# Kernel tuning notes

Hardware: AMD Instinct MI355X
Metric: run time of the kernel (lower is better)

Reference implementation:

```python
import jax, jax.numpy as jnp
import numpy as np

B, L, H, E = 2, 2048, 8, 64
S = L  # self-attention


def setup_inputs() -> dict:
    key = jax.random.key(0)
    k1, k2, k3, k4, k5 = jax.random.split(key, 5)
    return {
        "queries": jax.random.normal(k1, (B, L, H, E), dtype=jnp.float32),
        "keys": jax.random.normal(k2, (B, S, H, E), dtype=jnp.float32),
        "values": jax.random.normal(k3, (B, S, H, E), dtype=jnp.float32),
        "tau": jax.random.uniform(k4, (B, 1), dtype=jnp.float32),
        "delta": jax.random.normal(k5, (B, S), dtype=jnp.float32),
    }


def reference(queries, keys, values, tau, delta):
    # De-stationary attention: scores = (QK^T) * tau + delta, causal mask, softmax, AV
    E_ = queries.shape[-1]
    scale = 1.0 / jnp.sqrt(jnp.float32(E_))
    tau_b = tau[:, None, None, :]      # [B,1,1,1]
    delta_b = delta[:, None, None, :]  # [B,1,1,S]
    scores = jnp.einsum('blhe,bshe->bhls', queries, keys) * tau_b + delta_b  # [B,H,L,S]
    Lq, Sk = scores.shape[-2], scores.shape[-1]
    causal = jnp.triu(jnp.ones((Lq, Sk), dtype=bool), k=1)  # True = masked
    scores = jnp.where(causal[None, None], -jnp.inf, scores)
    A = jax.nn.softmax(scale * scores, axis=-1)
    V = jnp.einsum('bhls,bshd->blhd', A, values)
    return V
```

## Files before the change

### kernel.cpp

```cpp
#include <hip/hip_runtime.h>


typedef _Float16 h8 __attribute__((ext_vector_type(8)));
typedef _Float16 h2 __attribute__((ext_vector_type(2)));
typedef float f32x4 __attribute__((ext_vector_type(4)));

constexpr int Bc = 2, Lc = 2048, Hc = 8, Ec = 64, Sc = 2048;
constexpr int QTL = 128;
constexpr int NQT = Lc / QTL;
constexpr int KT = 64;
constexpr int LDK = 72;
constexpr float SCALE = 0.125f;
constexpr float LOG2E = 1.44269504088896340736f;

__device__ __forceinline__ h2 pk2(float x, float y) {
  return __builtin_bit_cast(h2, __builtin_amdgcn_cvt_pkrtz(x, y));
}
template <int CTRL>
__device__ __forceinline__ float dpp_f(float x) {
  int r = __builtin_amdgcn_update_dpp(0, __builtin_bit_cast(int, x), CTRL, 0xF, 0xF, true);
  return __builtin_bit_cast(float, r);
}
__device__ __forceinline__ float rowmax16(float x) {
  x = fmaxf(x, dpp_f<0xB1>(x));
  x = fmaxf(x, dpp_f<0x4E>(x));
  x = fmaxf(x, dpp_f<0x124>(x));
  x = fmaxf(x, dpp_f<0x128>(x));
  return x;
}

template <int CH_IT, int EPB>
__global__ __launch_bounds__(256, 2)
void dsattn_fwd(const float* __restrict__ Qg, const float* __restrict__ Kg,
                const float* __restrict__ Vg, const float* __restrict__ taug,
                const float* __restrict__ deltag, float* __restrict__ Og,
                _Float16* __restrict__ Opart, float* __restrict__ Mpart,
                float* __restrict__ Lpart) {
  __shared__ __align__(16) _Float16 Ks[2][KT * LDK];
  __shared__ __align__(16) _Float16 Vt[2][Ec * LDK];
  __shared__ __align__(16) _Float16 Pb[4][16 * LDK];

  int qt = NQT - 1, c0 = 0, pre_e = 0;
  if (CH_IT < 2 * NQT) {
    int bxx = (int)blockIdx.x;
#pragma unroll
    for (int q = NQT - 1; q >= 0; --q) {
      const int n = (2 * q + 1 + CH_IT) / CH_IT;
      if (bxx < n) { qt = q; c0 = bxx; break; }
      bxx -= n;
    }
#pragma unroll
    for (int q = 0; q < NQT; ++q)
      if (q < qt) pre_e += (2 * q + 1 + CH_IT) / CH_IT;
  } else {
    qt = NQT - 1 - (int)blockIdx.x;
  }
  const int ntiles = 2 * qt + 2;
  const int nch = (ntiles + CH_IT - 1) / CH_IT;
  const int ktBeg = c0 * CH_IT;
  const int ktEnd = min(ktBeg + CH_IT - 1, ntiles - 1);

  const int tid = threadIdx.x;
  const int wave = tid >> 6, lane = tid & 63;
  const int quad = lane >> 4, l16 = lane & 15;
  const int q0 = qt * QTL;
  const int bh = (int)blockIdx.y;
  const int b = bh >> 3, h = bh & 7;
  const float ct = taug[b] * (SCALE * LOG2E);

  h8 qfrag[2][2];
#pragma unroll
  for (int f = 0; f < 2; ++f)
#pragma unroll
    for (int kk = 0; kk < 2; ++kk) {
      const float* qp = Qg + (((size_t)b * Lc + q0 + 32 * wave + 16 * f + l16) * Hc + h) * Ec
                       + quad * 8 + kk * 32;
      const float4* p = (const float4*)qp;
      union { h8 v; h2 c[4]; } u;
      float4 a0 = p[0], a1 = p[1];
      u.c[0] = pk2(a0.x, a0.y); u.c[1] = pk2(a0.z, a0.w);
      u.c[2] = pk2(a1.x, a1.y); u.c[3] = pk2(a1.z, a1.w);
      qfrag[f][kk] = u.v;
    }

  h8 onesf;
#pragma unroll
  for (int j = 0; j < 8; ++j) onesf[j] = (_Float16)1.0f;

  f32x4 Oacc[2][4], Osum[2];
  float mrow[2][4];
#pragma unroll
  for (int f = 0; f < 2; ++f) {
#pragma unroll
    for (int nt = 0; nt < 4; ++nt) Oacc[f][nt] = (f32x4){0.f, 0.f, 0.f, 0.f};
    Osum[f] = (f32x4){0.f, 0.f, 0.f, 0.f};
#pragma unroll
    for (int r = 0; r < 4; ++r) mrow[f][r] = -1e30f;
  }

  const int srow = tid >> 2;
  const int sec = (tid & 3) << 4;
  const int vrp = ((tid >> 3) + 4 * (tid & 7)) & 31;
  const int ve8 = (tid & 7) << 3;

  _Float16* pb = &Pb[wave][0];
  const int lo = l16 & 1;
  const int pbase = (lo ? 32 : 0) + (l16 & ~1);
  float dcur[4];

  {
    const int kb = ktBeg * KT;
    const float* kp = Kg + (((size_t)b * Sc + kb + srow) * Hc + h) * Ec + sec;
    float4 c0v = ((const float4*)kp)[0], c1v = ((const float4*)kp)[1];
    float4 c2v = ((const float4*)kp)[2], c3v = ((const float4*)kp)[3];
    const float* vp0 = Vg + (((size_t)b * Sc + kb + 2 * vrp) * Hc + h) * Ec + ve8;
    const float* vp1 = vp0 + Hc * Ec;
    float4 r00 = ((const float4*)vp0)[0], r01 = ((const float4*)vp0)[1];
    float4 r10 = ((const float4*)vp1)[0], r11 = ((const float4*)vp1)[1];
#pragma unroll
    for (int nt = 0; nt < 4; ++nt)
      dcur[nt] = deltag[(size_t)b * Sc + kb + nt * 16 + l16] * (SCALE * LOG2E);
    union { h8 v; h2 c[4]; } w0, w1;
    w0.c[0] = pk2(c0v.x, c0v.y); w0.c[1] = pk2(c0v.z, c0v.w);
    w0.c[2] = pk2(c1v.x, c1v.y); w0.c[3] = pk2(c1v.z, c1v.w);
    w1.c[0] = pk2(c2v.x, c2v.y); w1.c[1] = pk2(c2v.z, c2v.w);
    w1.c[2] = pk2(c3v.x, c3v.y); w1.c[3] = pk2(c3v.z, c3v.w);
    *(h8*)&Ks[0][srow * LDK + sec] = w0.v;
    *(h8*)&Ks[0][srow * LDK + sec + 8] = w1.v;
    const float e0[8] = {r00.x, r00.y, r00.z, r00.w, r01.x, r01.y, r01.z, r01.w};
    const float e1[8] = {r10.x, r10.y, r10.z, r10.w, r11.x, r11.y, r11.z, r11.w};
#pragma unroll
    for (int j = 0; j < 8; ++j)
      *(h2*)&Vt[0][(ve8 + j) * LDK + 2 * vrp] = pk2(e0[j], e1[j]);
  }

  for (int kt = ktBeg; kt <= ktEnd; ++kt) {
    const int cur = (kt - ktBeg) & 1;
    const bool pf = (kt < ktEnd);
    const int kbase = kt * KT;

    __syncthreads();

    float4 kn0, kn1, kn2, kn3, vn00, vn01, vn10, vn11;
    float dn[4];
    if (pf) {
      const int nb = (kt + 1) * KT;
      const float* kp = Kg + (((size_t)b * Sc + nb + srow) * Hc + h) * Ec + sec;
      kn0 = ((const float4*)kp)[0]; kn1 = ((const float4*)kp)[1];
      kn2 = ((const float4*)kp)[2]; kn3 = ((const float4*)kp)[3];
      const float* vp0 = Vg + (((size_t)b * Sc + nb + 2 * vrp) * Hc + h) * Ec + ve8;
      const float* vp1 = vp0 + Hc * Ec;
      vn00 = ((const float4*)vp0)[0]; vn01 = ((const float4*)vp0)[1];
      vn10 = ((const float4*)vp1)[0]; vn11 = ((const float4*)vp1)[1];
#pragma unroll
      for (int nt = 0; nt < 4; ++nt)
        dn[nt] = deltag[(size_t)b * Sc + nb + nt * 16 + l16];
    }

    const int wtop = q0 + 32 * wave + 31;
    if (kbase <= wtop) {
      f32x4 Sacc[2][4];
#pragma unroll
      for (int f = 0; f < 2; ++f)
#pragma unroll
        for (int nt = 0; nt < 4; ++nt) Sacc[f][nt] = (f32x4){0.f, 0.f, 0.f, 0.f};
#pragma unroll
      for (int kk = 0; kk < 2; ++kk) {
        h8 bf[4];
#pragma unroll
        for (int nt = 0; nt < 4; ++nt)
          bf[nt] = *(const h8*)&Ks[cur][(nt * 16 + l16) * LDK + quad * 8 + kk * 32];
#pragma unroll
        for (int f = 0; f < 2; ++f)
#pragma unroll
          for (int nt = 0; nt < 4; ++nt)
            Sacc[f][nt] = __builtin_amdgcn_mfma_f32_16x16x32_f16(qfrag[f][kk], bf[nt], Sacc[f][nt], 0, 0, 0);
      }

#pragma unroll
      for (int f = 0; f < 2; ++f) {
        const int fr0 = q0 + 32 * wave + 16 * f;
        float sv[4][4];
#pragma unroll
        for (int nt = 0; nt < 4; ++nt)
#pragma unroll
          for (int r = 0; r < 4; ++r)
            sv[nt][r] = Sacc[f][nt][r] * ct + dcur[nt];
        if (kbase + 63 > fr0) {
#pragma unroll
          for (int nt = 0; nt < 4; ++nt) {
            const int key = kbase + nt * 16 + l16;
#pragma unroll
            for (int r = 0; r < 4; ++r)
              if (key > fr0 + quad * 4 + r) sv[nt][r] = -1e30f;
          }
        }
#pragma unroll
        for (int r = 0; r < 4; ++r) {
          float tm = fmaxf(fmaxf(sv[0][r], sv[1][r]), fmaxf(sv[2][r], sv[3][r]));
          tm = rowmax16(tm);
          float mn = fmaxf(mrow[f][r], tm);
          float alpha = __builtin_amdgcn_exp2f(mrow[f][r] - mn);
          mrow[f][r] = mn;
#pragma unroll
          for (int nt = 0; nt < 4; ++nt)
            sv[nt][r] = __builtin_amdgcn_exp2f(sv[nt][r] - mn);
          Osum[f][r] *= alpha;
#pragma unroll
          for (int nt = 0; nt < 4; ++nt) Oacc[f][nt][r] *= alpha;
        }
#pragma unroll
        for (int r = 0; r < 4; ++r) {
          float o0 = dpp_f<0xB1>(sv[0][r]);
          float o1 = dpp_f<0xB1>(sv[1][r]);
          float o2 = dpp_f<0xB1>(sv[2][r]);
          float o3 = dpp_f<0xB1>(sv[3][r]);
          h2 d0 = lo ? pk2(o2, sv[2][r]) : pk2(sv[0][r], o0);
          h2 d1 = lo ? pk2(o3, sv[3][r]) : pk2(sv[1][r], o1);
          _Float16* pp = &pb[((quad << 2) + r) * LDK + pbase];
          *(h2*)pp = d0;
          *(h2*)(pp + 16) = d1;
        }
        asm volatile("s_waitcnt lgkmcnt(0)" ::: "memory");

        h8 af0 = *(const h8*)&pb[l16 * LDK + quad * 8];
        h8 af1 = *(const h8*)&pb[l16 * LDK + quad * 8 + 32];

#pragma unroll
        for (int nt = 0; nt < 4; ++nt) {
          h8 vf0 = *(const h8*)&Vt[cur][(nt * 16 + l16) * LDK + quad * 8];
          Oacc[f][nt] = __builtin_amdgcn_mfma_f32_16x16x32_f16(af0, vf0, Oacc[f][nt], 0, 0, 0);
          h8 vf1 = *(const h8*)&Vt[cur][(nt * 16 + l16) * LDK + quad * 8 + 32];
          Oacc[f][nt] = __builtin_amdgcn_mfma_f32_16x16x32_f16(af1, vf1, Oacc[f][nt], 0, 0, 0);
        }
        Osum[f] = __builtin_amdgcn_mfma_f32_16x16x32_f16(af0, onesf, Osum[f], 0, 0, 0);
        Osum[f] = __builtin_amdgcn_mfma_f32_16x16x32_f16(af1, onesf, Osum[f], 0, 0, 0);
      }
    }

    if (pf) {
      _Float16* ksn = &Ks[cur ^ 1][0];
      _Float16* vtn = &Vt[cur ^ 1][0];
      union { h8 v; h2 c[4]; } w0, w1;
      w0.c[0] = pk2(kn0.x, kn0.y); w0.c[1] = pk2(kn0.z, kn0.w);
      w0.c[2] = pk2(kn1.x, kn1.y); w0.c[3] = pk2(kn1.z, kn1.w);
      w1.c[0] = pk2(kn2.x, kn2.y); w1.c[1] = pk2(kn2.z, kn2.w);
      w1.c[2] = pk2(kn3.x, kn3.y); w1.c[3] = pk2(kn3.z, kn3.w);
      *(h8*)&ksn[srow * LDK + sec] = w0.v;
      *(h8*)&ksn[srow * LDK + sec + 8] = w1.v;
      const float e0[8] = {vn00.x, vn00.y, vn00.z, vn00.w, vn01.x, vn01.y, vn01.z, vn01.w};
      const float e1[8] = {vn10.x, vn10.y, vn10.z, vn10.w, vn11.x, vn11.y, vn11.z, vn11.w};
#pragma unroll
      for (int j = 0; j < 8; ++j)
        *(h2*)&vtn[(ve8 + j) * LDK + 2 * vrp] = pk2(e0[j], e1[j]);
#pragma unroll
      for (int nt = 0; nt < 4; ++nt) dcur[nt] = dn[nt] * (SCALE * LOG2E);
    }
  }

  if (nch == 1) {
#pragma unroll
    for (int f = 0; f < 2; ++f)
#pragma unroll
      for (int r = 0; r < 4; ++r) {
        const int qrow = q0 + 32 * wave + 16 * f + (quad << 2) + r;
        const float inv = 1.0f / Osum[f][r];
        float* op = Og + (((size_t)b * Lc + qrow) * Hc + h) * Ec;
#pragma unroll
        for (int nt = 0; nt < 4; ++nt) op[nt * 16 + l16] = Oacc[f][nt][r] * inv;
      }
  } else {
    const int e = bh * EPB + pre_e + c0;
    _Float16* op = Opart + (size_t)e * (QTL * Ec);
#pragma unroll
    for (int f = 0; f < 2; ++f)
#pragma unroll
      for (int r = 0; r < 4; ++r) {
        const int row = 32 * wave + 16 * f + (quad << 2) + r;
#pragma unroll
        for (int nt = 0; nt < 4; ++nt)
          op[row * Ec + nt * 16 + l16] = (_Float16)Oacc[f][nt][r];
        if (l16 == 0) {
          Mpart[e * QTL + row] = mrow[f][r];
          Lpart[e * QTL + row] = Osum[f][r];
        }
      }
  }
}

template <int CH_IT, int EPB>
__global__ __launch_bounds__(256, 4)
void dsattn_comb(const _Float16* __restrict__ Opart, const float* __restrict__ Mpart,
                 const float* __restrict__ Lpart, float* __restrict__ Og) {
  const int qt = (CH_IT / 2) + ((int)blockIdx.x >> 2);
  const int slab = (int)blockIdx.x & 3;
  const int bh = (int)blockIdx.y;
  const int b = bh >> 3, h = bh & 7;
  const int nch = (2 * qt + 1 + CH_IT) / CH_IT;
  int pre_e = 0;
#pragma unroll
  for (int q = 0; q < NQT; ++q)
    if (q < qt) pre_e += (2 * q + 1 + CH_IT) / CH_IT;
  const int e0 = bh * EPB + pre_e;

  const int row = slab * 32 + ((int)threadIdx.x >> 3);
  const int col = ((int)threadIdx.x & 7) << 3;

  float ms[8];
  float M = -1e30f;
  for (int c = 0; c < nch; ++c) {
    ms[c] = Mpart[(e0 + c) * QTL + row];
    M = fmaxf(M, ms[c]);
  }
  float acc[8];
#pragma unroll
  for (int i = 0; i < 8; ++i) acc[i] = 0.f;
  float l = 0.f;
  for (int c = 0; c < nch; ++c) {
    const float w = __builtin_amdgcn_exp2f(ms[c] - M);
    l += w * Lpart[(e0 + c) * QTL + row];
    h8 v = *(const h8*)(Opart + (size_t)(e0 + c) * (QTL * Ec) + row * Ec + col);
#pragma unroll
    for (int i = 0; i < 8; ++i) acc[i] += w * (float)v[i];
  }
  const float inv = 1.0f / l;
  float* out = Og + (((size_t)b * Lc + qt * QTL + row) * Hc + h) * Ec + col;
  float4 o0, o1;
  o0.x = acc[0] * inv; o0.y = acc[1] * inv; o0.z = acc[2] * inv; o0.w = acc[3] * inv;
  o1.x = acc[4] * inv; o1.y = acc[5] * inv; o1.z = acc[6] * inv; o1.w = acc[7] * inv;
  ((float4*)out)[0] = o0;
  ((float4*)out)[1] = o1;
}

extern "C" void kernel_launch(void* const* d_in, const int* in_sizes, int n_in,
                              void* d_out, int out_size, void* d_ws, size_t ws_size,
                              hipStream_t stream) {
  const float* Q = (const float*)d_in[0];
  const float* K = (const float*)d_in[1];
  const float* V = (const float*)d_in[2];
  const float* tau = (const float*)d_in[3];
  const float* delta = (const float*)d_in[4];
  float* O = (float*)d_out;

  constexpr int CH = 4;
  constexpr int EPB = 72;
  constexpr int TOT_E = Bc * Hc * EPB;
  const size_t need = (size_t)TOT_E * QTL * Ec * 2 + 2 * (size_t)TOT_E * QTL * 4;

  if (ws_size >= need) {
    _Float16* Opart = (_Float16*)d_ws;
    float* Mpart = (float*)(Opart + (size_t)TOT_E * QTL * Ec);
    float* Lpart = Mpart + (size_t)TOT_E * QTL;
    dim3 g1(EPB, Bc * Hc);
    dsattn_fwd<CH, EPB><<<g1, 256, 0, stream>>>(Q, K, V, tau, delta, O,
                                                Opart, Mpart, Lpart);
    dim3 g2((NQT - CH / 2) * 4, Bc * Hc);
    dsattn_comb<CH, EPB><<<g2, 256, 0, stream>>>(Opart, Mpart, Lpart, O);
  } else {
    dim3 g1(NQT, Bc * Hc);
    dsattn_fwd<32, 1><<<g1, 256, 0, stream>>>(Q, K, V, tau, delta, O,
                                              nullptr, nullptr, nullptr);
  }
}
```

Before: 118.6 us.

## Double query tile to 256 rows with 512-thread blocks sharing K/V tiles

Raises the query tile from 128 to 256 rows and runs 8 waves per block, so each K/V tile staged into LDS serves twice as many query rows. The cooperative K/V load is split across 512 threads, each handling half as much data, and the split-K chunk bookkeeping and combine grid are re-derived for the new tile count. The aim is to cut redundant global K/V loads and fp16 conversion per query row. In exchange there are half as many blocks, larger causal-diagonal waste per tile, and higher per-block register and LDS pressure.

```diff
diff --git a/kernel.cpp b/kernel.cpp
--- a/kernel.cpp
+++ b/kernel.cpp
@@ -6,7 +6,7 @@
 typedef float f32x4 __attribute__((ext_vector_type(4)));
 
 constexpr int Bc = 2, Lc = 2048, Hc = 8, Ec = 64, Sc = 2048;
-constexpr int QTL = 128;
+constexpr int QTL = 256;
 constexpr int NQT = Lc / QTL;
 constexpr int KT = 64;
 constexpr int LDK = 72;
@@ -30,7 +30,7 @@
 }
 
 template <int CH_IT, int EPB>
-__global__ __launch_bounds__(256, 2)
+__global__ __launch_bounds__(512, 2)
 void dsattn_fwd(const float* __restrict__ Qg, const float* __restrict__ Kg,
                 const float* __restrict__ Vg, const float* __restrict__ taug,
                 const float* __restrict__ deltag, float* __restrict__ Og,
@@ -38,24 +38,24 @@
                 float* __restrict__ Lpart) {
   __shared__ __align__(16) _Float16 Ks[2][KT * LDK];
   __shared__ __align__(16) _Float16 Vt[2][Ec * LDK];
-  __shared__ __align__(16) _Float16 Pb[4][16 * LDK];
+  __shared__ __align__(16) _Float16 Pb[8][16 * LDK];
 
   int qt = NQT - 1, c0 = 0, pre_e = 0;
-  if (CH_IT < 2 * NQT) {
+  if (CH_IT < 4 * NQT) {
     int bxx = (int)blockIdx.x;
 #pragma unroll
     for (int q = NQT - 1; q >= 0; --q) {
-      const int n = (2 * q + 1 + CH_IT) / CH_IT;
+      const int n = (4 * q + 3 + CH_IT) / CH_IT;
       if (bxx < n) { qt = q; c0 = bxx; break; }
       bxx -= n;
     }
 #pragma unroll
     for (int q = 0; q < NQT; ++q)
-      if (q < qt) pre_e += (2 * q + 1 + CH_IT) / CH_IT;
+      if (q < qt) pre_e += (4 * q + 3 + CH_IT) / CH_IT;
   } else {
     qt = NQT - 1 - (int)blockIdx.x;
   }
-  const int ntiles = 2 * qt + 2;
+  const int ntiles = 4 * qt + 4;
   const int nch = (ntiles + CH_IT - 1) / CH_IT;
   const int ktBeg = c0 * CH_IT;
   const int ktEnd = min(ktBeg + CH_IT - 1, ntiles - 1);
@@ -98,10 +98,10 @@
     for (int r = 0; r < 4; ++r) mrow[f][r] = -1e30f;
   }
 
-  const int srow = tid >> 2;
-  const int sec = (tid & 3) << 4;
-  const int vrp = ((tid >> 3) + 4 * (tid & 7)) & 31;
-  const int ve8 = (tid & 7) << 3;
+  const int srow = tid >> 3;
+  const int sec = (tid & 7) << 3;
+  const int vrp = ((tid >> 4) + 2 * (tid & 15)) & 31;
+  const int ve4 = (tid & 15) << 2;
 
   _Float16* pb = &Pb[wave][0];
   const int lo = l16 & 1;
@@ -112,26 +112,22 @@
     const int kb = ktBeg * KT;
     const float* kp = Kg + (((size_t)b * Sc + kb + srow) * Hc + h) * Ec + sec;
     float4 c0v = ((const float4*)kp)[0], c1v = ((const float4*)kp)[1];
-    float4 c2v = ((const float4*)kp)[2], c3v = ((const float4*)kp)[3];
-    const float* vp0 = Vg + (((size_t)b * Sc + kb + 2 * vrp) * Hc + h) * Ec + ve8;
+    const float* vp0 = Vg + (((size_t)b * Sc + kb + 2 * vrp) * Hc + h) * Ec + ve4;
     const float* vp1 = vp0 + Hc * Ec;
-    float4 r00 = ((const float4*)vp0)[0], r01 = ((const float4*)vp0)[1];
-    float4 r10 = ((const float4*)vp1)[0], r11 = ((const float4*)vp1)[1];
+    float4 r0 = *(const float4*)vp0;
+    float4 r1 = *(const float4*)vp1;
 #pragma unroll
     for (int nt = 0; nt < 4; ++nt)
       dcur[nt] = deltag[(size_t)b * Sc + kb + nt * 16 + l16] * (SCALE * LOG2E);
-    union { h8 v; h2 c[4]; } w0, w1;
+    union { h8 v; h2 c[4]; } w0;
     w0.c[0] = pk2(c0v.x, c0v.y); w0.c[1] = pk2(c0v.z, c0v.w);
     w0.c[2] = pk2(c1v.x, c1v.y); w0.c[3] = pk2(c1v.z, c1v.w);
-    w1.c[0] = pk2(c2v.x, c2v.y); w1.c[1] = pk2(c2v.z, c2v.w);
-    w1.c[2] = pk2(c3v.x, c3v.y); w1.c[3] = pk2(c3v.z, c3v.w);
     *(h8*)&Ks[0][srow * LDK + sec] = w0.v;
-    *(h8*)&Ks[0][srow * LDK + sec + 8] = w1.v;
-    const float e0[8] = {r00.x, r00.y, r00.z, r00.w, r01.x, r01.y, r01.z, r01.w};
-    const float e1[8] = {r10.x, r10.y, r10.z, r10.w, r11.x, r11.y, r11.z, r11.w};
-#pragma unroll
-    for (int j = 0; j < 8; ++j)
-      *(h2*)&Vt[0][(ve8 + j) * LDK + 2 * vrp] = pk2(e0[j], e1[j]);
+    const float e0[4] = {r0.x, r0.y, r0.z, r0.w};
+    const float e1[4] = {r1.x, r1.y, r1.z, r1.w};
+#pragma unroll
+    for (int j = 0; j < 4; ++j)
+      *(h2*)&Vt[0][(ve4 + j) * LDK + 2 * vrp] = pk2(e0[j], e1[j]);
   }
 
   for (int kt = ktBeg; kt <= ktEnd; ++kt) {
@@ -141,17 +137,16 @@
 
     __syncthreads();
 
-    float4 kn0, kn1, kn2, kn3, vn00, vn01, vn10, vn11;
+    float4 kn0, kn1, vn0, vn1;
     float dn[4];
     if (pf) {
       const int nb = (kt + 1) * KT;
       const float* kp = Kg + (((size_t)b * Sc + nb + srow) * Hc + h) * Ec + sec;
       kn0 = ((const float4*)kp)[0]; kn1 = ((const float4*)kp)[1];
-      kn2 = ((const float4*)kp)[2]; kn3 = ((const float4*)kp)[3];
-      const float* vp0 = Vg + (((size_t)b * Sc + nb + 2 * vrp) * Hc + h) * Ec + ve8;
+      const float* vp0 = Vg + (((size_t)b * Sc + nb + 2 * vrp) * Hc + h) * Ec + ve4;
       const float* vp1 = vp0 + Hc * Ec;
-      vn00 = ((const float4*)vp0)[0]; vn01 = ((const float4*)vp0)[1];
-      vn10 = ((const float4*)vp1)[0]; vn11 = ((const float4*)vp1)[1];
+      vn0 = *(const float4*)vp0;
+      vn1 = *(const float4*)vp1;
 #pragma unroll
       for (int nt = 0; nt < 4; ++nt)
         dn[nt] = deltag[(size_t)b * Sc + nb + nt * 16 + l16];
@@ -241,18 +236,15 @@
     if (pf) {
       _Float16* ksn = &Ks[cur ^ 1][0];
       _Float16* vtn = &Vt[cur ^ 1][0];
-      union { h8 v; h2 c[4]; } w0, w1;
+      union { h8 v; h2 c[4]; } w0;
       w0.c[0] = pk2(kn0.x, kn0.y); w0.c[1] = pk2(kn0.z, kn0.w);
       w0.c[2] = pk2(kn1.x, kn1.y); w0.c[3] = pk2(kn1.z, kn1.w);
-      w1.c[0] = pk2(kn2.x, kn2.y); w1.c[1] = pk2(kn2.z, kn2.w);
-      w1.c[2] = pk2(kn3.x, kn3.y); w1.c[3] = pk2(kn3.z, kn3.w);
       *(h8*)&ksn[srow * LDK + sec] = w0.v;
-      *(h8*)&ksn[srow * LDK + sec + 8] = w1.v;
-      const float e0[8] = {vn00.x, vn00.y, vn00.z, vn00.w, vn01.x, vn01.y, vn01.z, vn01.w};
-      const float e1[8] = {vn10.x, vn10.y, vn10.z, vn10.w, vn11.x, vn11.y, vn11.z, vn11.w};
-#pragma unroll
-      for (int j = 0; j < 8; ++j)
-        *(h2*)&vtn[(ve8 + j) * LDK + 2 * vrp] = pk2(e0[j], e1[j]);
+      const float e0[4] = {vn0.x, vn0.y, vn0.z, vn0.w};
+      const float e1[4] = {vn1.x, vn1.y, vn1.z, vn1.w};
+#pragma unroll
+      for (int j = 0; j < 4; ++j)
+        *(h2*)&vtn[(ve4 + j) * LDK + 2 * vrp] = pk2(e0[j], e1[j]);
 #pragma unroll
       for (int nt = 0; nt < 4; ++nt) dcur[nt] = dn[nt] * (SCALE * LOG2E);
     }
@@ -292,15 +284,15 @@
 __global__ __launch_bounds__(256, 4)
 void dsattn_comb(const _Float16* __restrict__ Opart, const float* __restrict__ Mpart,
                  const float* __restrict__ Lpart, float* __restrict__ Og) {
-  const int qt = (CH_IT / 2) + ((int)blockIdx.x >> 2);
-  const int slab = (int)blockIdx.x & 3;
+  const int qt = 1 + ((int)blockIdx.x >> 3);
+  const int slab = (int)blockIdx.x & 7;
   const int bh = (int)blockIdx.y;
   const int b = bh >> 3, h = bh & 7;
-  const int nch = (2 * qt + 1 + CH_IT) / CH_IT;
+  const int nch = (4 * qt + 3 + CH_IT) / CH_IT;
   int pre_e = 0;
 #pragma unroll
   for (int q = 0; q < NQT; ++q)
-    if (q < qt) pre_e += (2 * q + 1 + CH_IT) / CH_IT;
+    if (q < qt) pre_e += (4 * q + 3 + CH_IT) / CH_IT;
   const int e0 = bh * EPB + pre_e;
 
   const int row = slab * 32 + ((int)threadIdx.x >> 3);
@@ -343,7 +335,7 @@
   float* O = (float*)d_out;
 
   constexpr int CH = 4;
-  constexpr int EPB = 72;
+  constexpr int EPB = 36;
   constexpr int TOT_E = Bc * Hc * EPB;
   const size_t need = (size_t)TOT_E * QTL * Ec * 2 + 2 * (size_t)TOT_E * QTL * 4;
 
@@ -352,13 +344,13 @@
     float* Mpart = (float*)(Opart + (size_t)TOT_E * QTL * Ec);
     float* Lpart = Mpart + (size_t)TOT_E * QTL;
     dim3 g1(EPB, Bc * Hc);
-    dsattn_fwd<CH, EPB><<<g1, 256, 0, stream>>>(Q, K, V, tau, delta, O,
+    dsattn_fwd<CH, EPB><<<g1, 512, 0, stream>>>(Q, K, V, tau, delta, O,
                                                 Opart, Mpart, Lpart);
-    dim3 g2((NQT - CH / 2) * 4, Bc * Hc);
+    dim3 g2((NQT - 1) * 8, Bc * Hc);
     dsattn_comb<CH, EPB><<<g2, 256, 0, stream>>>(Opart, Mpart, Lpart, O);
   } else {
     dim3 g1(NQT, Bc * Hc);
-    dsattn_fwd<32, 1><<<g1, 256, 0, stream>>>(Q, K, V, tau, delta, O,
+    dsattn_fwd<32, 1><<<g1, 512, 0, stream>>>(Q, K, V, tau, delta, O,
                                               nullptr, nullptr, nullptr);
   }
 }
```

New measurement: 123.8 us. +4.4%, slower.

## Convert forward attention kernel to persistent grid with strided work-item loop

Applied to the files above, without the earlier changes.

The forward kernel now launches a fixed grid of 768 blocks. Each block loops over work items (bh, chunk) striding by gridDim, with bh as the fastest index so heads interleave and the heaviest query tiles are scheduled first. The aim is to even out load across CUs for the causal triangular workload and to cut block launch overhead. The cost is an extra __syncthreads per item, repeated per-item setup, and a loss of natural one-block-per-slot scheduling if 768 does not match the device's resident capacity.

```diff
diff --git a/kernel.cpp b/kernel.cpp
--- a/kernel.cpp
+++ b/kernel.cpp
@@ -10,6 +10,7 @@
 constexpr int NQT = Lc / QTL;
 constexpr int KT = 64;
 constexpr int LDK = 72;
+constexpr int NBH = Bc * Hc;
 constexpr float SCALE = 0.125f;
 constexpr float LOG2E = 1.44269504088896340736f;
 
@@ -29,7 +30,7 @@
   return x;
 }
 
-template <int CH_IT, int EPB>
+template <int CH_IT, int EPB, int NIT>
 __global__ __launch_bounds__(256, 2)
 void dsattn_fwd(const float* __restrict__ Qg, const float* __restrict__ Kg,
                 const float* __restrict__ Vg, const float* __restrict__ taug,
@@ -40,251 +41,250 @@
   __shared__ __align__(16) _Float16 Vt[2][Ec * LDK];
   __shared__ __align__(16) _Float16 Pb[4][16 * LDK];
 
-  int qt = NQT - 1, c0 = 0, pre_e = 0;
-  if (CH_IT < 2 * NQT) {
-    int bxx = (int)blockIdx.x;
-#pragma unroll
-    for (int q = NQT - 1; q >= 0; --q) {
-      const int n = (2 * q + 1 + CH_IT) / CH_IT;
-      if (bxx < n) { qt = q; c0 = bxx; break; }
-      bxx -= n;
-    }
-#pragma unroll
-    for (int q = 0; q < NQT; ++q)
-      if (q < qt) pre_e += (2 * q + 1 + CH_IT) / CH_IT;
-  } else {
-    qt = NQT - 1 - (int)blockIdx.x;
-  }
-  const int ntiles = 2 * qt + 2;
-  const int nch = (ntiles + CH_IT - 1) / CH_IT;
-  const int ktBeg = c0 * CH_IT;
-  const int ktEnd = min(ktBeg + CH_IT - 1, ntiles - 1);
-
   const int tid = threadIdx.x;
   const int wave = tid >> 6, lane = tid & 63;
   const int quad = lane >> 4, l16 = lane & 15;
-  const int q0 = qt * QTL;
-  const int bh = (int)blockIdx.y;
-  const int b = bh >> 3, h = bh & 7;
-  const float ct = taug[b] * (SCALE * LOG2E);
-
-  h8 qfrag[2][2];
-#pragma unroll
-  for (int f = 0; f < 2; ++f)
-#pragma unroll
-    for (int kk = 0; kk < 2; ++kk) {
-      const float* qp = Qg + (((size_t)b * Lc + q0 + 32 * wave + 16 * f + l16) * Hc + h) * Ec
-                       + quad * 8 + kk * 32;
-      const float4* p = (const float4*)qp;
-      union { h8 v; h2 c[4]; } u;
-      float4 a0 = p[0], a1 = p[1];
-      u.c[0] = pk2(a0.x, a0.y); u.c[1] = pk2(a0.z, a0.w);
-      u.c[2] = pk2(a1.x, a1.y); u.c[3] = pk2(a1.z, a1.w);
-      qfrag[f][kk] = u.v;
-    }
-
-  h8 onesf;
-#pragma unroll
-  for (int j = 0; j < 8; ++j) onesf[j] = (_Float16)1.0f;
-
-  f32x4 Oacc[2][4], Osum[2];
-  float mrow[2][4];
-#pragma unroll
-  for (int f = 0; f < 2; ++f) {
-#pragma unroll
-    for (int nt = 0; nt < 4; ++nt) Oacc[f][nt] = (f32x4){0.f, 0.f, 0.f, 0.f};
-    Osum[f] = (f32x4){0.f, 0.f, 0.f, 0.f};
-#pragma unroll
-    for (int r = 0; r < 4; ++r) mrow[f][r] = -1e30f;
-  }
-
   const int srow = tid >> 2;
   const int sec = (tid & 3) << 4;
   const int vrp = ((tid >> 3) + 4 * (tid & 7)) & 31;
   const int ve8 = (tid & 7) << 3;
-
   _Float16* pb = &Pb[wave][0];
   const int lo = l16 & 1;
   const int pbase = (lo ? 32 : 0) + (l16 & ~1);
-  float dcur[4];
-
-  {
-    const int kb = ktBeg * KT;
-    const float* kp = Kg + (((size_t)b * Sc + kb + srow) * Hc + h) * Ec + sec;
-    float4 c0v = ((const float4*)kp)[0], c1v = ((const float4*)kp)[1];
-    float4 c2v = ((const float4*)kp)[2], c3v = ((const float4*)kp)[3];
-    const float* vp0 = Vg + (((size_t)b * Sc + kb + 2 * vrp) * Hc + h) * Ec + ve8;
-    const float* vp1 = vp0 + Hc * Ec;
-    float4 r00 = ((const float4*)vp0)[0], r01 = ((const float4*)vp0)[1];
-    float4 r10 = ((const float4*)vp1)[0], r11 = ((const float4*)vp1)[1];
-#pragma unroll
-    for (int nt = 0; nt < 4; ++nt)
-      dcur[nt] = deltag[(size_t)b * Sc + kb + nt * 16 + l16] * (SCALE * LOG2E);
-    union { h8 v; h2 c[4]; } w0, w1;
-    w0.c[0] = pk2(c0v.x, c0v.y); w0.c[1] = pk2(c0v.z, c0v.w);
-    w0.c[2] = pk2(c1v.x, c1v.y); w0.c[3] = pk2(c1v.z, c1v.w);
-    w1.c[0] = pk2(c2v.x, c2v.y); w1.c[1] = pk2(c2v.z, c2v.w);
-    w1.c[2] = pk2(c3v.x, c3v.y); w1.c[3] = pk2(c3v.z, c3v.w);
-    *(h8*)&Ks[0][srow * LDK + sec] = w0.v;
-    *(h8*)&Ks[0][srow * LDK + sec + 8] = w1.v;
-    const float e0[8] = {r00.x, r00.y, r00.z, r00.w, r01.x, r01.y, r01.z, r01.w};
-    const float e1[8] = {r10.x, r10.y, r10.z, r10.w, r11.x, r11.y, r11.z, r11.w};
-#pragma unroll
-    for (int j = 0; j < 8; ++j)
-      *(h2*)&Vt[0][(ve8 + j) * LDK + 2 * vrp] = pk2(e0[j], e1[j]);
-  }
-
-  for (int kt = ktBeg; kt <= ktEnd; ++kt) {
-    const int cur = (kt - ktBeg) & 1;
-    const bool pf = (kt < ktEnd);
-    const int kbase = kt * KT;
+
+  h8 onesf;
+#pragma unroll
+  for (int j = 0; j < 8; ++j) onesf[j] = (_Float16)1.0f;
+
+  for (int wid = (int)blockIdx.x; wid < NIT; wid += (int)gridDim.x) {
+    const int bh = wid & (NBH - 1);
+    const int e = wid >> 4;
+    int qt = NQT - 1, c0 = 0, pre_e = 0;
+    {
+      int ee = e, acc = 0;
+#pragma unroll
+      for (int q = NQT - 1; q >= 0; --q) {
+        const int n = (2 * q + 1 + CH_IT) / CH_IT;
+        if (ee < n) { qt = q; c0 = ee; pre_e = EPB - acc - n; break; }
+        ee -= n; acc += n;
+      }
+    }
+    const int ntiles = 2 * qt + 2;
+    const int nch = (ntiles + CH_IT - 1) / CH_IT;
+    const int ktBeg = c0 * CH_IT;
+    const int ktEnd = min(ktBeg + CH_IT - 1, ntiles - 1);
+    const int q0 = qt * QTL;
+    const int b = bh >> 3, h = bh & 7;
+    const float ct = taug[b] * (SCALE * LOG2E);
+
+    h8 qfrag[2][2];
+#pragma unroll
+    for (int f = 0; f < 2; ++f)
+#pragma unroll
+      for (int kk = 0; kk < 2; ++kk) {
+        const float* qp = Qg + (((size_t)b * Lc + q0 + 32 * wave + 16 * f + l16) * Hc + h) * Ec
+                         + quad * 8 + kk * 32;
+        const float4* p = (const float4*)qp;
+        union { h8 v; h2 c[4]; } u;
+        float4 a0 = p[0], a1 = p[1];
+        u.c[0] = pk2(a0.x, a0.y); u.c[1] = pk2(a0.z, a0.w);
+        u.c[2] = pk2(a1.x, a1.y); u.c[3] = pk2(a1.z, a1.w);
+        qfrag[f][kk] = u.v;
+      }
+
+    f32x4 Oacc[2][4], Osum[2];
+    float mrow[2][4];
+#pragma unroll
+    for (int f = 0; f < 2; ++f) {
+#pragma unroll
+      for (int nt = 0; nt < 4; ++nt) Oacc[f][nt] = (f32x4){0.f, 0.f, 0.f, 0.f};
+      Osum[f] = (f32x4){0.f, 0.f, 0.f, 0.f};
+#pragma unroll
+      for (int r = 0; r < 4; ++r) mrow[f][r] = -1e30f;
+    }
+
+    float dcur[4];
 
     __syncthreads();
 
-    float4 kn0, kn1, kn2, kn3, vn00, vn01, vn10, vn11;
-    float dn[4];
-    if (pf) {
-      const int nb = (kt + 1) * KT;
-      const float* kp = Kg + (((size_t)b * Sc + nb + srow) * Hc + h) * Ec + sec;
-      kn0 = ((const float4*)kp)[0]; kn1 = ((const float4*)kp)[1];
-      kn2 = ((const float4*)kp)[2]; kn3 = ((const float4*)kp)[3];
-      const float* vp0 = Vg + (((size_t)b * Sc + nb + 2 * vrp) * Hc + h) * Ec + ve8;
+    {
+      const int kb = ktBeg * KT;
+      const float* kp = Kg + (((size_t)b * Sc + kb + srow) * Hc + h) * Ec + sec;
+      float4 c0v = ((const float4*)kp)[0], c1v = ((const float4*)kp)[1];
+      float4 c2v = ((const float4*)kp)[2], c3v = ((const float4*)kp)[3];
+      const float* vp0 = Vg + (((size_t)b * Sc + kb + 2 * vrp) * Hc + h) * Ec + ve8;
       const float* vp1 = vp0 + Hc * Ec;
-      vn00 = ((const float4*)vp0)[0]; vn01 = ((const float4*)vp0)[1];
-      vn10 = ((const float4*)vp1)[0]; vn11 = ((const float4*)vp1)[1];
+      float4 r00 = ((const float4*)vp0)[0], r01 = ((const float4*)vp0)[1];
+      float4 r10 = ((const float4*)vp1)[0], r11 = ((const float4*)vp1)[1];
 #pragma unroll
       for (int nt = 0; nt < 4; ++nt)
-        dn[nt] = deltag[(size_t)b * Sc + nb + nt * 16 + l16];
-    }
-
-    const int wtop = q0 + 32 * wave + 31;
-    if (kbase <= wtop) {
-      f32x4 Sacc[2][4];
+        dcur[nt] = deltag[(size_t)b * Sc + kb + nt * 16 + l16] * (SCALE * LOG2E);
+      union { h8 v; h2 c[4]; } w0, w1;
+      w0.c[0] = pk2(c0v.x, c0v.y); w0.c[1] = pk2(c0v.z, c0v.w);
+      w0.c[2] = pk2(c1v.x, c1v.y); w0.c[3] = pk2(c1v.z, c1v.w);
+      w1.c[0] = pk2(c2v.x, c2v.y); w1.c[1] = pk2(c2v.z, c2v.w);
+      w1.c[2] = pk2(c3v.x, c3v.y); w1.c[3] = pk2(c3v.z, c3v.w);
+      *(h8*)&Ks[0][srow * LDK + sec] = w0.v;
+      *(h8*)&Ks[0][srow * LDK + sec + 8] = w1.v;
+      const float e0[8] = {r00.x, r00.y, r00.z, r00.w, r01.x, r01.y, r01.z, r01.w};
+      const float e1[8] = {r10.x, r10.y, r10.z, r10.w, r11.x, r11.y, r11.z, r11.w};
+#pragma unroll
+      for (int j = 0; j < 8; ++j)
+        *(h2*)&Vt[0][(ve8 + j) * LDK + 2 * vrp] = pk2(e0[j], e1[j]);
+    }
+
+    for (int kt = ktBeg; kt <= ktEnd; ++kt) {
+      const int cur = (kt - ktBeg) & 1;
+      const bool pf = (kt < ktEnd);
+      const int kbase = kt * KT;
+
+      __syncthreads();
+
+      float4 kn0, kn1, kn2, kn3, vn00, vn01, vn10, vn11;
+      float dn[4];
+      if (pf) {
+        const int nb = (kt + 1) * KT;
+        const float* kp = Kg + (((size_t)b * Sc + nb + srow) * Hc + h) * Ec + sec;
+        kn0 = ((const float4*)kp)[0]; kn1 = ((const float4*)kp)[1];
+        kn2 = ((const float4*)kp)[2]; kn3 = ((const float4*)kp)[3];
+        const float* vp0 = Vg + (((size_t)b * Sc + nb + 2 * vrp) * Hc + h) * Ec + ve8;
+        const float* vp1 = vp0 + Hc * Ec;
+        vn00 = ((const float4*)vp0)[0]; vn01 = ((const float4*)vp0)[1];
+        vn10 = ((const float4*)vp1)[0]; vn11 = ((const float4*)vp1)[1];
+#pragma unroll
+        for (int nt = 0; nt < 4; ++nt)
+          dn[nt] = deltag[(size_t)b * Sc + nb + nt * 16 + l16];
+      }
+
+      const int wtop = q0 + 32 * wave + 31;
+      if (kbase <= wtop) {
+        f32x4 Sacc[2][4];
+#pragma unroll
+        for (int f = 0; f < 2; ++f)
+#pragma unroll
+          for (int nt = 0; nt < 4; ++nt) Sacc[f][nt] = (f32x4){0.f, 0.f, 0.f, 0.f};
+#pragma unroll
+        for (int kk = 0; kk < 2; ++kk) {
+          h8 bf[4];
+#pragma unroll
+          for (int nt = 0; nt < 4; ++nt)
+            bf[nt] = *(const h8*)&Ks[cur][(nt * 16 + l16) * LDK + quad * 8 + kk * 32];
+#pragma unroll
+          for (int f = 0; f < 2; ++f)
+#pragma unroll
+            for (int nt = 0; nt < 4; ++nt)
+              Sacc[f][nt] = __builtin_amdgcn_mfma_f32_16x16x32_f16(qfrag[f][kk], bf[nt], Sacc[f][nt], 0, 0, 0);
+        }
+
+#pragma unroll
+        for (int f = 0; f < 2; ++f) {
+          const int fr0 = q0 + 32 * wave + 16 * f;
+          float sv[4][4];
+#pragma unroll
+          for (int nt = 0; nt < 4; ++nt)
+#pragma unroll
+            for (int r = 0; r < 4; ++r)
+              sv[nt][r] = Sacc[f][nt][r] * ct + dcur[nt];
+          if (kbase + 63 > fr0) {
+#pragma unroll
+            for (int nt = 0; nt < 4; ++nt) {
+              const int key = kbase + nt * 16 + l16;
+#pragma unroll
+              for (int r = 0; r < 4; ++r)
+                if (key > fr0 + quad * 4 + r) sv[nt][r] = -1e30f;
+            }
+          }
+#pragma unroll
+          for (int r = 0; r < 4; ++r) {
+            float tm = fmaxf(fmaxf(sv[0][r], sv[1][r]), fmaxf(sv[2][r], sv[3][r]));
+            tm = rowmax16(tm);
+            float mn = fmaxf(mrow[f][r], tm);
+            float alpha = __builtin_amdgcn_exp2f(mrow[f][r] - mn);
+            mrow[f][r] = mn;
+#pragma unroll
+            for (int nt = 0; nt < 4; ++nt)
+              sv[nt][r] = __builtin_amdgcn_exp2f(sv[nt][r] - mn);
+            Osum[f][r] *= alpha;
+#pragma unroll
+            for (int nt = 0; nt < 4; ++nt) Oacc[f][nt][r] *= alpha;
+          }
+#pragma unroll
+          for (int r = 0; r < 4; ++r) {
+            float o0 = dpp_f<0xB1>(sv[0][r]);
+            float o1 = dpp_f<0xB1>(sv[1][r]);
+            float o2 = dpp_f<0xB1>(sv[2][r]);
+            float o3 = dpp_f<0xB1>(sv[3][r]);
+            h2 d0 = lo ? pk2(o2, sv[2][r]) : pk2(sv[0][r], o0);
+            h2 d1 = lo ? pk2(o3, sv[3][r]) : pk2(sv[1][r], o1);
+            _Float16* pp = &pb[((quad << 2) + r) * LDK + pbase];
+            *(h2*)pp = d0;
+            *(h2*)(pp + 16) = d1;
+          }
+          asm volatile("s_waitcnt lgkmcnt(0)" ::: "memory");
+
+          h8 af0 = *(const h8*)&pb[l16 * LDK + quad * 8];
+          h8 af1 = *(const h8*)&pb[l16 * LDK + quad * 8 + 32];
+
+#pragma unroll
+          for (int nt = 0; nt < 4; ++nt) {
+            h8 vf0 = *(const h8*)&Vt[cur][(nt * 16 + l16) * LDK + quad * 8];
+            Oacc[f][nt] = __builtin_amdgcn_mfma_f32_16x16x32_f16(af0, vf0, Oacc[f][nt], 0, 0, 0);
+            h8 vf1 = *(const h8*)&Vt[cur][(nt * 16 + l16) * LDK + quad * 8 + 32];
+            Oacc[f][nt] = __builtin_amdgcn_mfma_f32_16x16x32_f16(af1, vf1, Oacc[f][nt], 0, 0, 0);
+          }
+          Osum[f] = __builtin_amdgcn_mfma_f32_16x16x32_f16(af0, onesf, Osum[f], 0, 0, 0);
+          Osum[f] = __builtin_amdgcn_mfma_f32_16x16x32_f16(af1, onesf, Osum[f], 0, 0, 0);
+        }
+      }
+
+      if (pf) {
+        _Float16* ksn = &Ks[cur ^ 1][0];
+        _Float16* vtn = &Vt[cur ^ 1][0];
+        union { h8 v; h2 c[4]; } w0, w1;
+        w0.c[0] = pk2(kn0.x, kn0.y); w0.c[1] = pk2(kn0.z, kn0.w);
+        w0.c[2] = pk2(kn1.x, kn1.y); w0.c[3] = pk2(kn1.z, kn1.w);
+        w1.c[0] = pk2(kn2.x, kn2.y); w1.c[1] = pk2(kn2.z, kn2.w);
+        w1.c[2] = pk2(kn3.x, kn3.y); w1.c[3] = pk2(kn3.z, kn3.w);
+        *(h8*)&ksn[srow * LDK + sec] = w0.v;
+        *(h8*)&ksn[srow * LDK + sec + 8] = w1.v;
+        const float e0[8] = {vn00.x, vn00.y, vn00.z, vn00.w, vn01.x, vn01.y, vn01.z, vn01.w};
+        const float e1[8] = {vn10.x, vn10.y, vn10.z, vn10.w, vn11.x, vn11.y, vn11.z, vn11.w};
+#pragma unroll
+        for (int j = 0; j < 8; ++j)
+          *(h2*)&vtn[(ve8 + j) * LDK + 2 * vrp] = pk2(e0[j], e1[j]);
+#pragma unroll
+        for (int nt = 0; nt < 4; ++nt) dcur[nt] = dn[nt] * (SCALE * LOG2E);
+      }
+    }
+
+    if (nch == 1) {
 #pragma unroll
       for (int f = 0; f < 2; ++f)
 #pragma unroll
-        for (int nt = 0; nt < 4; ++nt) Sacc[f][nt] = (f32x4){0.f, 0.f, 0.f, 0.f};
-#pragma unroll
-      for (int kk = 0; kk < 2; ++kk) {
-        h8 bf[4];
-#pragma unroll
-        for (int nt = 0; nt < 4; ++nt)
-          bf[nt] = *(const h8*)&Ks[cur][(nt * 16 + l16) * LDK + quad * 8 + kk * 32];
-#pragma unroll
-        for (int f = 0; f < 2; ++f)
+        for (int r = 0; r < 4; ++r) {
+          const int qrow = q0 + 32 * wave + 16 * f + (quad << 2) + r;
+          const float inv = 1.0f / Osum[f][r];
+          float* op = Og + (((size_t)b * Lc + qrow) * Hc + h) * Ec;
+#pragma unroll
+          for (int nt = 0; nt < 4; ++nt) op[nt * 16 + l16] = Oacc[f][nt][r] * inv;
+        }
+    } else {
+      const int en = bh * EPB + pre_e + c0;
+      _Float16* op = Opart + (size_t)en * (QTL * Ec);
+#pragma unroll
+      for (int f = 0; f < 2; ++f)
+#pragma unroll
+        for (int r = 0; r < 4; ++r) {
+          const int row = 32 * wave + 16 * f + (quad << 2) + r;
 #pragma unroll
           for (int nt = 0; nt < 4; ++nt)
-            Sacc[f][nt] = __builtin_amdgcn_mfma_f32_16x16x32_f16(qfrag[f][kk], bf[nt], Sacc[f][nt], 0, 0, 0);
-      }
-
-#pragma unroll
-      for (int f = 0; f < 2; ++f) {
-        const int fr0 = q0 + 32 * wave + 16 * f;
-        float sv[4][4];
-#pragma unroll
-        for (int nt = 0; nt < 4; ++nt)
-#pragma unroll
-          for (int r = 0; r < 4; ++r)
-            sv[nt][r] = Sacc[f][nt][r] * ct + dcur[nt];
-        if (kbase + 63 > fr0) {
-#pragma unroll
-          for (int nt = 0; nt < 4; ++nt) {
-            const int key = kbase + nt * 16 + l16;
-#pragma unroll
-            for (int r = 0; r < 4; ++r)
-              if (key > fr0 + quad * 4 + r) sv[nt][r] = -1e30f;
+            op[row * Ec + nt * 16 + l16] = (_Float16)Oacc[f][nt][r];
+          if (l16 == 0) {
+            Mpart[en * QTL + row] = mrow[f][r];
+            Lpart[en * QTL + row] = Osum[f][r];
           }
         }
-#pragma unroll
-        for (int r = 0; r < 4; ++r) {
-          float tm = fmaxf(fmaxf(sv[0][r], sv[1][r]), fmaxf(sv[2][r], sv[3][r]));
-          tm = rowmax16(tm);
-          float mn = fmaxf(mrow[f][r], tm);
-          float alpha = __builtin_amdgcn_exp2f(mrow[f][r] - mn);
-          mrow[f][r] = mn;
-#pragma unroll
-          for (int nt = 0; nt < 4; ++nt)
-            sv[nt][r] = __builtin_amdgcn_exp2f(sv[nt][r] - mn);
-          Osum[f][r] *= alpha;
-#pragma unroll
-          for (int nt = 0; nt < 4; ++nt) Oacc[f][nt][r] *= alpha;
-        }
-#pragma unroll
-        for (int r = 0; r < 4; ++r) {
-          float o0 = dpp_f<0xB1>(sv[0][r]);
-          float o1 = dpp_f<0xB1>(sv[1][r]);
-          float o2 = dpp_f<0xB1>(sv[2][r]);
-          float o3 = dpp_f<0xB1>(sv[3][r]);
-          h2 d0 = lo ? pk2(o2, sv[2][r]) : pk2(sv[0][r], o0);
-          h2 d1 = lo ? pk2(o3, sv[3][r]) : pk2(sv[1][r], o1);
-          _Float16* pp = &pb[((quad << 2) + r) * LDK + pbase];
-          *(h2*)pp = d0;
-          *(h2*)(pp + 16) = d1;
-        }
-        asm volatile("s_waitcnt lgkmcnt(0)" ::: "memory");
-
-        h8 af0 = *(const h8*)&pb[l16 * LDK + quad * 8];
-        h8 af1 = *(const h8*)&pb[l16 * LDK + quad * 8 + 32];
-
-#pragma unroll
-        for (int nt = 0; nt < 4; ++nt) {
-          h8 vf0 = *(const h8*)&Vt[cur][(nt * 16 + l16) * LDK + quad * 8];
-          Oacc[f][nt] = __builtin_amdgcn_mfma_f32_16x16x32_f16(af0, vf0, Oacc[f][nt], 0, 0, 0);
-          h8 vf1 = *(const h8*)&Vt[cur][(nt * 16 + l16) * LDK + quad * 8 + 32];
-          Oacc[f][nt] = __builtin_amdgcn_mfma_f32_16x16x32_f16(af1, vf1, Oacc[f][nt], 0, 0, 0);
-        }
-        Osum[f] = __builtin_amdgcn_mfma_f32_16x16x32_f16(af0, onesf, Osum[f], 0, 0, 0);
-        Osum[f] = __builtin_amdgcn_mfma_f32_16x16x32_f16(af1, onesf, Osum[f], 0, 0, 0);
-      }
-    }
-
-    if (pf) {
-      _Float16* ksn = &Ks[cur ^ 1][0];
-      _Float16* vtn = &Vt[cur ^ 1][0];
-      union { h8 v; h2 c[4]; } w0, w1;
-      w0.c[0] = pk2(kn0.x, kn0.y); w0.c[1] = pk2(kn0.z, kn0.w);
-      w0.c[2] = pk2(kn1.x, kn1.y); w0.c[3] = pk2(kn1.z, kn1.w);
-      w1.c[0] = pk2(kn2.x, kn2.y); w1.c[1] = pk2(kn2.z, kn2.w);
-      w1.c[2] = pk2(kn3.x, kn3.y); w1.c[3] = pk2(kn3.z, kn3.w);
-      *(h8*)&ksn[srow * LDK + sec] = w0.v;
-      *(h8*)&ksn[srow * LDK + sec + 8] = w1.v;
-      const float e0[8] = {vn00.x, vn00.y, vn00.z, vn00.w, vn01.x, vn01.y, vn01.z, vn01.w};
-      const float e1[8] = {vn10.x, vn10.y, vn10.z, vn10.w, vn11.x, vn11.y, vn11.z, vn11.w};
-#pragma unroll
-      for (int j = 0; j < 8; ++j)
-        *(h2*)&vtn[(ve8 + j) * LDK + 2 * vrp] = pk2(e0[j], e1[j]);
-#pragma unroll
-      for (int nt = 0; nt < 4; ++nt) dcur[nt] = dn[nt] * (SCALE * LOG2E);
-    }
-  }
-
-  if (nch == 1) {
-#pragma unroll
-    for (int f = 0; f < 2; ++f)
-#pragma unroll
-      for (int r = 0; r < 4; ++r) {
-        const int qrow = q0 + 32 * wave + 16 * f + (quad << 2) + r;
-        const float inv = 1.0f / Osum[f][r];
-        float* op = Og + (((size_t)b * Lc + qrow) * Hc + h) * Ec;
-#pragma unroll
-        for (int nt = 0; nt < 4; ++nt) op[nt * 16 + l16] = Oacc[f][nt][r] * inv;
-      }
-  } else {
-    const int e = bh * EPB + pre_e + c0;
-    _Float16* op = Opart + (size_t)e * (QTL * Ec);
-#pragma unroll
-    for (int f = 0; f < 2; ++f)
-#pragma unroll
-      for (int r = 0; r < 4; ++r) {
-        const int row = 32 * wave + 16 * f + (quad << 2) + r;
-#pragma unroll
-        for (int nt = 0; nt < 4; ++nt)
-          op[row * Ec + nt * 16 + l16] = (_Float16)Oacc[f][nt][r];
-        if (l16 == 0) {
-          Mpart[e * QTL + row] = mrow[f][r];
-          Lpart[e * QTL + row] = Osum[f][r];
-        }
-      }
+    }
   }
 }
 
@@ -345,20 +345,19 @@
   constexpr int CH = 4;
   constexpr int EPB = 72;
   constexpr int TOT_E = Bc * Hc * EPB;
+  constexpr int PERS = 768;
   const size_t need = (size_t)TOT_E * QTL * Ec * 2 + 2 * (size_t)TOT_E * QTL * 4;
 
   if (ws_size >= need) {
     _Float16* Opart = (_Float16*)d_ws;
     float* Mpart = (float*)(Opart + (size_t)TOT_E * QTL * Ec);
     float* Lpart = Mpart + (size_t)TOT_E * QTL;
-    dim3 g1(EPB, Bc * Hc);
-    dsattn_fwd<CH, EPB><<<g1, 256, 0, stream>>>(Q, K, V, tau, delta, O,
-                                                Opart, Mpart, Lpart);
+    dsattn_fwd<CH, EPB, TOT_E><<<dim3(PERS), 256, 0, stream>>>(
+        Q, K, V, tau, delta, O, Opart, Mpart, Lpart);
     dim3 g2((NQT - CH / 2) * 4, Bc * Hc);
     dsattn_comb<CH, EPB><<<g2, 256, 0, stream>>>(Opart, Mpart, Lpart, O);
   } else {
-    dim3 g1(NQT, Bc * Hc);
-    dsattn_fwd<32, 1><<<g1, 256, 0, stream>>>(Q, K, V, tau, delta, O,
-                                              nullptr, nullptr, nullptr);
+    dsattn_fwd<32, NQT, NQT * NBH><<<dim3(NQT * NBH), 256, 0, stream>>>(
+        Q, K, V, tau, delta, O, nullptr, nullptr, nullptr);
   }
 }
```

After: 115.8 us. 2.4% less time.
